# Optimization experiments

Hardware: AMD Instinct MI355X
Metric: run time of the kernel (lower is better)

## Reference

```python
import jax, jax.numpy as jnp
import numpy as np
import math

B, S, N_UNITS, D_K = 8, 2048, 1024, 512


def setup_inputs() -> dict:
    key = jax.random.key(0)
    ks = jax.random.split(key, 8)
    scale = 1.0 / math.sqrt(N_UNITS)
    query = jax.random.normal(ks[0], (B, S, N_UNITS), dtype=jnp.float32)
    k_in = jax.random.normal(ks[1], (B, S, N_UNITS), dtype=jnp.float32)
    v_in = jax.random.normal(ks[2], (B, S, N_UNITS), dtype=jnp.float32)
    # custom multiplicative mask: causal lower-triangular, broadcast over batch
    mask = jnp.broadcast_to(jnp.tril(jnp.ones((S, S), dtype=jnp.float32)), (B, S, S))
    Wq = jax.random.normal(ks[3], (N_UNITS, D_K), dtype=jnp.float32) * scale
    Wk = jax.random.normal(ks[4], (N_UNITS, D_K), dtype=jnp.float32) * scale
    Wv = jax.random.normal(ks[5], (N_UNITS, D_K), dtype=jnp.float32) * scale
    bq = jnp.zeros((D_K,), dtype=jnp.float32)
    bk = jnp.zeros((D_K,), dtype=jnp.float32)
    bv = jnp.zeros((D_K,), dtype=jnp.float32)
    return {"query": query, "key": k_in, "value": v_in, "mask": mask,
            "Wq": Wq, "bq": bq, "Wk": Wk, "bk": bk, "Wv": Wv, "bv": bv}


def reference(query, key, value, mask, Wq, bq, Wk, bk, Wv, bv):
    d_k = Wq.shape[-1]
    Q = jnp.einsum('bsn,nd->bsd', query, Wq) + bq  # [B,S,Dk]
    K = jnp.einsum('bsn,nd->bsd', key, Wk) + bk
    V = jnp.einsum('bsn,nd->bsd', value, Wv) + bv
    # scores [B,S,S]
    x_hat = jnp.einsum('bqd,bkd->bqk', Q, K) / jnp.sqrt(jnp.float32(d_k))
    # custom multiplicative mask: x*mask - 1e9*(1-mask)
    x_hat_masked = x_hat * mask - 1e9 * (1.0 - mask)
    attn = jax.nn.softmax(x_hat_masked, axis=-1)
    # dropout = 0.0 (eval mode) -> identity
    out = jnp.einsum('bqk,bkd->bqd', attn, V)
    return out
```

## Files before the change

### kernel.cpp

```cpp
#include <hip/hip_runtime.h>

typedef __bf16 bf16_t;
typedef __attribute__((ext_vector_type(4))) __bf16 bf16x4;
typedef __attribute__((ext_vector_type(8))) __bf16 bf16x8;
typedef __attribute__((ext_vector_type(4))) float f32x4;

#define B_    8
#define S_    2048
#define NU    1024
#define DK    512
#define MROWS (B_ * S_)
#define PBATCH (128 * 128 * 136)

#define WAITVM(N) asm volatile("s_waitcnt vmcnt(" #N ")" ::: "memory")
#define WAITLG    asm volatile("s_waitcnt lgkmcnt(0)" ::: "memory")
#define BAR       asm volatile("s_barrier" ::: "memory")

__device__ __forceinline__ f32x4 mfma16(bf16x8 a, bf16x8 b, f32x4 c) {
  return __builtin_amdgcn_mfma_f32_16x16x32_bf16(a, b, c, 0, 0, 0);
}

__device__ __forceinline__ void async_load16(const void* g, void* l) {
  __builtin_amdgcn_global_load_lds(
      (const __attribute__((address_space(1))) unsigned int*)g,
      (__attribute__((address_space(3))) unsigned int*)l, 16, 0, 0);
}

__device__ __forceinline__ bf16x8 cvt8(f32x4 x0, f32x4 x1) {
  bf16x8 r;
#pragma unroll
  for (int j = 0; j < 4; ++j) { r[j] = (bf16_t)x0[j]; r[j + 4] = (bf16_t)x1[j]; }
  return r;
}

__device__ __forceinline__ void stage_tile(const bf16_t* __restrict__ src,
                                           int rstride, bf16_t* dst, int k0,
                                           int tid) {
#pragma unroll
  for (int j = 0; j < 2; ++j) {
    const int g = j * 256 + tid;
    const int ln = g >> 3, c = g & 7;
    const int cs = c ^ (ln & 7);
    const int srow = 2 * ln + (cs >> 2);
    async_load16(src + (size_t)srow * rstride + k0 + (cs & 3) * 8, dst + g * 8);
  }
}

__device__ __forceinline__ void stage_tile_f32(const float* __restrict__ src,
                                               int rstride, float* dst, int k0,
                                               int tid) {
#pragma unroll
  for (int j = 0; j < 4; ++j) {
    const int g = j * 256 + tid;
    const int row = g >> 3, c = g & 7;
    const int cs = c ^ (row & 7);
    async_load16(src + (size_t)row * rstride + k0 + (cs << 2), dst + g * 4);
  }
}

__device__ __forceinline__ bf16x8 frag(const bf16_t* buf, int row, int q) {
  const int ln = row >> 1;
  const int cp = (((row & 1) << 2) | q) ^ (ln & 7);
  return *(const bf16x8*)(buf + ln * 64 + cp * 8);
}

__device__ __forceinline__ bf16x8 frag_f32(const float* buf, int row, int q) {
  const int s = row & 7;
  const f32x4 x0 = *(const f32x4*)&buf[row * 32 + (((q * 2)) ^ s) * 4];
  const f32x4 x1 = *(const f32x4*)&buf[row * 32 + (((q * 2) | 1) ^ s) * 4];
  return cvt8(x0, x1);
}

__global__ __launch_bounds__(256) void transpose_w_kernel(
    const float* __restrict__ Wq, const float* __restrict__ Wk,
    const float* __restrict__ Wv, bf16_t* __restrict__ Wt) {
  const float* W = (blockIdx.z == 0) ? Wq : (blockIdx.z == 1) ? Wk : Wv;
  bf16_t* Wo = Wt + (size_t)blockIdx.z * DK * NU;
  __shared__ float tile[32][33];
  const int t = threadIdx.x;
  const int r = t >> 5, c = t & 31;
  const int kbase = blockIdx.y * 32, nbase = blockIdx.x * 32;
#pragma unroll
  for (int i = 0; i < 4; ++i)
    tile[r + i * 8][c] = W[(size_t)(kbase + r + i * 8) * DK + nbase + c];
  __syncthreads();
#pragma unroll
  for (int i = 0; i < 4; ++i)
    Wo[(size_t)(nbase + r + i * 8) * NU + kbase + c] = (bf16_t)tile[c][r + i * 8];
}

__global__ __launch_bounds__(256, 2) void xw3_gemm_kernel(
    const float* __restrict__ q_in, const float* __restrict__ k_in,
    const float* __restrict__ v_in, const bf16_t* __restrict__ Wt,
    const float* __restrict__ bq, const float* __restrict__ bk,
    const float* __restrict__ bv, bf16_t* __restrict__ Qo,
    bf16_t* __restrict__ Ko, bf16_t* __restrict__ Vt) {
  const int bx = blockIdx.x;
  const int z = bx >> 9;
  const int t = bx & 511;
  const int m0 = (t & 127) * 128;
  const int n0 = (t >> 7) * 128;
  const float* X = (z == 0) ? q_in : (z == 1) ? k_in : v_in;
  const float* bias = (z == 0) ? bq : (z == 1) ? bk : bv;

  const int tid = threadIdx.x;
  const int wave = tid >> 6, lane = tid & 63;
  const int l16 = lane & 15, quad = lane >> 4;
  const int wm = (wave >> 1) * 64, wn = (wave & 1) * 64;

  __shared__ __align__(16) unsigned char smem[73728];
  float* ldsA = (float*)smem;
  bf16_t* ldsB = (bf16_t*)(smem + 49152);

  const float* Ag = X + (size_t)m0 * NU;
  const bf16_t* Bg = Wt + (size_t)z * DK * NU + (size_t)n0 * NU;

  f32x4 acc[4][4] = {};

  stage_tile_f32(Ag, NU, ldsA, 0, tid);
  stage_tile(Bg, NU, ldsB, 0, tid);
  stage_tile_f32(Ag, NU, ldsA + 4096, 32, tid);
  stage_tile(Bg, NU, ldsB + 4096, 32, tid);
  const int NS = 32;
  int cur = 0, nxt2 = 2;
  for (int ks = 0; ks < NS; ++ks) {
    if (ks + 1 < NS) { WAITVM(6); } else { WAITVM(0); }
    BAR;
    if (ks + 2 < NS) {
      stage_tile_f32(Ag, NU, ldsA + nxt2 * 4096, (ks + 2) * 32, tid);
      stage_tile(Bg, NU, ldsB + nxt2 * 4096, (ks + 2) * 32, tid);
    }
    const float* ac = ldsA + cur * 4096;
    const bf16_t* bc = ldsB + cur * 4096;
    bf16x8 af[4], bfr[4];
#pragma unroll
    for (int i = 0; i < 4; ++i) af[i] = frag_f32(ac, wm + i * 16 + l16, quad);
#pragma unroll
    for (int j = 0; j < 4; ++j) bfr[j] = frag(bc, wn + j * 16 + l16, quad);
#pragma unroll
    for (int i = 0; i < 4; ++i)
#pragma unroll
      for (int j = 0; j < 4; ++j)
        acc[i][j] = mfma16(af[i], bfr[j], acc[i][j]);
    cur = (cur + 1 == 3) ? 0 : cur + 1;
    nxt2 = (nxt2 + 1 == 3) ? 0 : nxt2 + 1;
  }

  if (z != 2) {
    bf16_t* Out = (z == 0) ? Qo : Ko;
#pragma unroll
    for (int j = 0; j < 4; ++j) {
      const int cn = n0 + wn + j * 16 + l16;
      const float bz = bias[cn];
#pragma unroll
      for (int i = 0; i < 4; ++i) {
        const int rm = m0 + wm + i * 16 + quad * 4;
#pragma unroll
        for (int r = 0; r < 4; ++r)
          Out[(size_t)(rm + r) * DK + cn] = (bf16_t)(acc[i][j][r] + bz);
      }
    }
  } else {
    bf16_t* Ts = (bf16_t*)smem;
    BAR;
#pragma unroll
    for (int j = 0; j < 4; ++j) {
      const int cnl = wn + j * 16 + l16;
      const float bz = bias[n0 + cnl];
#pragma unroll
      for (int i = 0; i < 4; ++i) {
        const int rs = wm + i * 16 + quad * 4;
        bf16x4 tv;
#pragma unroll
        for (int r = 0; r < 4; ++r) tv[r] = (bf16_t)(acc[i][j][r] + bz);
        *(bf16x4*)&Ts[cnl * 136 + rs] = tv;
      }
    }
    WAITLG; BAR;
    const int bb2 = m0 >> 11, sl = m0 & 2047;
    const int row = tid >> 1, half = tid & 1;
    bf16_t* dst = Vt + ((size_t)bb2 * DK + n0 + row) * S_ + sl + half * 64;
    const bf16_t* sp = &Ts[row * 136 + half * 64];
#pragma unroll
    for (int k = 0; k < 8; ++k)
      *(bf16x8*)(dst + k * 8) = *(const bf16x8*)(sp + k * 8);
  }
}

__global__ __launch_bounds__(256) void zerol_kernel(float* __restrict__ L) {
  ((f32x4*)L)[blockIdx.x * 256 + threadIdx.x] = f32x4{0.f, 0.f, 0.f, 0.f};
}

__global__ __launch_bounds__(256, 3) void qk_p_kernel(
    const bf16_t* __restrict__ Q, const bf16_t* __restrict__ K,
    bf16_t* __restrict__ P, float* __restrict__ L) {
  const int bx = blockIdx.x;
  const int b = bx & 7;
  const int t = bx >> 3;
  int mt = 0;
  while (((mt + 1) * (mt + 2)) / 2 <= t) ++mt;
  const int nt = t - (mt * (mt + 1)) / 2;
  const int klen = (mt + 1) * 128;

  const int tid = threadIdx.x;
  const int wave = tid >> 6, lane = tid & 63;
  const int l16 = lane & 15, quad = lane >> 4;
  const int wm = (wave >> 1) * 64, wn = (wave & 1) * 64;

  __shared__ __align__(16) unsigned char smem[49152];
  bf16_t* lds = (bf16_t*)smem;

  const bf16_t* Ag = Q + (size_t)(b * S_ + mt * 128) * DK;
  const bf16_t* Bg = K + (size_t)(b * S_ + nt * 128) * DK;

  f32x4 acc[4][4] = {};

  stage_tile(Ag, DK, lds, 0, tid);
  stage_tile(Bg, DK, lds + 12288, 0, tid);
  stage_tile(Ag, DK, lds + 4096, 32, tid);
  stage_tile(Bg, DK, lds + 16384, 32, tid);
  const int NS = 16;
  int cur = 0, nxt2 = 2;
  for (int ks = 0; ks < NS; ++ks) {
    if (ks + 1 < NS) { WAITVM(4); } else { WAITVM(0); }
    BAR;
    if (ks + 2 < NS) {
      stage_tile(Ag, DK, lds + nxt2 * 4096, (ks + 2) * 32, tid);
      stage_tile(Bg, DK, lds + 12288 + nxt2 * 4096, (ks + 2) * 32, tid);
    }
    const bf16_t* ac = lds + cur * 4096;
    const bf16_t* bc = lds + 12288 + cur * 4096;
    bf16x8 af[4], bfr[4];
#pragma unroll
    for (int i = 0; i < 4; ++i) af[i] = frag(ac, wm + i * 16 + l16, quad);
#pragma unroll
    for (int j = 0; j < 4; ++j) bfr[j] = frag(bc, wn + j * 16 + l16, quad);
#pragma unroll
    for (int i = 0; i < 4; ++i)
#pragma unroll
      for (int j = 0; j < 4; ++j)
        acc[i][j] = mfma16(af[i], bfr[j], acc[i][j]);
    cur = (cur + 1 == 3) ? 0 : cur + 1;
    nxt2 = (nxt2 + 1 == 3) ? 0 : nxt2 + 1;
  }

  const float scale = 0.04419417382415922f;
  bf16_t* Pt = P + (size_t)b * PBATCH + (size_t)8192 * mt * (mt + 1);
  float* Lb = L + b * S_ + mt * 128;
#pragma unroll
  for (int i = 0; i < 4; ++i) {
#pragma unroll
    for (int r = 0; r < 4; ++r) {
      const int lrow = wm + i * 16 + quad * 4 + r;
      const int srow = mt * 128 + lrow;
      float rsum = 0.f;
#pragma unroll
      for (int j = 0; j < 4; ++j) {
        const int scol = nt * 128 + wn + j * 16 + l16;
        const float p =
            (scol > srow) ? 0.f : __expf(acc[i][j][r] * scale - 10.0f);
        rsum += p;
        Pt[(size_t)lrow * klen + scol] = (bf16_t)p;
      }
#pragma unroll
      for (int off = 8; off >= 1; off >>= 1)
        rsum += __shfl_xor(rsum, off, 64);
      if (l16 == 0) atomicAdd(&Lb[lrow], rsum);
    }
  }
}

__global__ __launch_bounds__(256, 3) void pv_kernel(
    const bf16_t* __restrict__ P, const bf16_t* __restrict__ Vt,
    const float* __restrict__ L, float* __restrict__ Out) {
  const int bx = blockIdx.x;
  const int b = bx & 7;
  const int u = bx >> 3;
  const int mt = 15 - (u >> 2);
  const int d0 = (u & 3) * 128;
  const int klen = (mt + 1) * 128;
  const int NS = (mt + 1) * 4;

  const int tid = threadIdx.x;
  const int wave = tid >> 6, lane = tid & 63;
  const int l16 = lane & 15, quad = lane >> 4;
  const int wm = (wave >> 1) * 64, wn = (wave & 1) * 64;

  __shared__ __align__(16) unsigned char smem[49152];
  bf16_t* lds = (bf16_t*)smem;

  const bf16_t* Ag = P + (size_t)b * PBATCH + (size_t)8192 * mt * (mt + 1);
  const bf16_t* Bg = Vt + ((size_t)b * DK + d0) * S_;

  f32x4 acc[4][4] = {};

  stage_tile(Ag, klen, lds, 0, tid);
  stage_tile(Bg, S_, lds + 12288, 0, tid);
  stage_tile(Ag, klen, lds + 4096, 32, tid);
  stage_tile(Bg, S_, lds + 16384, 32, tid);
  int cur = 0, nxt2 = 2;
  for (int ks = 0; ks < NS; ++ks) {
    if (ks + 1 < NS) { WAITVM(4); } else { WAITVM(0); }
    BAR;
    if (ks + 2 < NS) {
      stage_tile(Ag, klen, lds + nxt2 * 4096, (ks + 2) * 32, tid);
      stage_tile(Bg, S_, lds + 12288 + nxt2 * 4096, (ks + 2) * 32, tid);
    }
    const bf16_t* ac = lds + cur * 4096;
    const bf16_t* bc = lds + 12288 + cur * 4096;
    bf16x8 af[4], bfr[4];
#pragma unroll
    for (int i = 0; i < 4; ++i) af[i] = frag(ac, wm + i * 16 + l16, quad);
#pragma unroll
    for (int j = 0; j < 4; ++j) bfr[j] = frag(bc, wn + j * 16 + l16, quad);
#pragma unroll
    for (int i = 0; i < 4; ++i)
#pragma unroll
      for (int j = 0; j < 4; ++j)
        acc[i][j] = mfma16(af[i], bfr[j], acc[i][j]);
    cur = (cur + 1 == 3) ? 0 : cur + 1;
    nxt2 = (nxt2 + 1 == 3) ? 0 : nxt2 + 1;
  }

  const int m0 = b * S_ + mt * 128;
#pragma unroll
  for (int i = 0; i < 4; ++i) {
#pragma unroll
    for (int r = 0; r < 4; ++r) {
      const int grow = m0 + wm + i * 16 + quad * 4 + r;
      const float inv = 1.0f / L[grow];
      float* orow = Out + (size_t)grow * DK + d0;
#pragma unroll
      for (int j = 0; j < 4; ++j)
        orow[wn + j * 16 + l16] = acc[i][j][r] * inv;
    }
  }
}

extern "C" void kernel_launch(void* const* d_in, const int* in_sizes, int n_in,
                              void* d_out, int out_size, void* d_ws, size_t ws_size,
                              hipStream_t stream) {
  const float* query = (const float*)d_in[0];
  const float* key_i = (const float*)d_in[1];
  const float* value = (const float*)d_in[2];
  const float* Wq = (const float*)d_in[4];
  const float* bq = (const float*)d_in[5];
  const float* Wk = (const float*)d_in[6];
  const float* bk = (const float*)d_in[7];
  const float* Wv = (const float*)d_in[8];
  const float* bv = (const float*)d_in[9];
  float* out = (float*)d_out;

  bf16_t* Wt = (bf16_t*)d_ws;
  bf16_t* Qw = Wt + (size_t)3 * DK * NU;
  bf16_t* Kw = Qw + (size_t)MROWS * DK;
  bf16_t* Vw = Kw + (size_t)MROWS * DK;
  bf16_t* Pw = Vw + (size_t)MROWS * DK;
  float* Lw = (float*)(Pw + (size_t)B_ * PBATCH);

  transpose_w_kernel<<<dim3(16, 32, 3), 256, 0, stream>>>(Wq, Wk, Wv, Wt);
  zerol_kernel<<<16, 256, 0, stream>>>(Lw);
  xw3_gemm_kernel<<<1536, 256, 0, stream>>>(query, key_i, value, Wt, bq, bk,
                                            bv, Qw, Kw, Vw);
  qk_p_kernel<<<1088, 256, 0, stream>>>(Qw, Kw, Pw, Lw);
  pv_kernel<<<512, 256, 0, stream>>>(Pw, Vw, Lw, out);
}
```

Before: 440.9 us.

## Switch GEMMs to double buffering for occupancy and replace atomic row-sum with partials

All three GEMM kernels drop from triple-buffered LDS staging (prefetch depth two) to double buffering (prefetch depth one). This shrinks shared memory so launch bounds can allow one more block per CU. Separately, the softmax row-sum atomics and the zeroing kernel are replaced by per-tile partial sums written to workspace, which pv_kernel reduces into LDS before normalising. The risk is that the shallower prefetch now waits on vmcnt(0) every step, exposing more memory latency per iteration.

New measurement: 444.0 us. Within noise of the previous version (+0.7%).

```diff
diff --git a/kernel.cpp b/kernel.cpp
--- a/kernel.cpp
+++ b/kernel.cpp
@@ -89,7 +89,7 @@
     Wo[(size_t)(nbase + r + i * 8) * NU + kbase + c] = (bf16_t)tile[c][r + i * 8];
 }
 
-__global__ __launch_bounds__(256, 2) void xw3_gemm_kernel(
+__global__ __launch_bounds__(256, 3) void xw3_gemm_kernel(
     const float* __restrict__ q_in, const float* __restrict__ k_in,
     const float* __restrict__ v_in, const bf16_t* __restrict__ Wt,
     const float* __restrict__ bq, const float* __restrict__ bk,
@@ -108,9 +108,9 @@
   const int l16 = lane & 15, quad = lane >> 4;
   const int wm = (wave >> 1) * 64, wn = (wave & 1) * 64;
 
-  __shared__ __align__(16) unsigned char smem[73728];
+  __shared__ __align__(16) unsigned char smem[49152];
   float* ldsA = (float*)smem;
-  bf16_t* ldsB = (bf16_t*)(smem + 49152);
+  bf16_t* ldsB = (bf16_t*)(smem + 32768);
 
   const float* Ag = X + (size_t)m0 * NU;
   const bf16_t* Bg = Wt + (size_t)z * DK * NU + (size_t)n0 * NU;
@@ -119,19 +119,16 @@
 
   stage_tile_f32(Ag, NU, ldsA, 0, tid);
   stage_tile(Bg, NU, ldsB, 0, tid);
-  stage_tile_f32(Ag, NU, ldsA + 4096, 32, tid);
-  stage_tile(Bg, NU, ldsB + 4096, 32, tid);
   const int NS = 32;
-  int cur = 0, nxt2 = 2;
   for (int ks = 0; ks < NS; ++ks) {
-    if (ks + 1 < NS) { WAITVM(6); } else { WAITVM(0); }
+    WAITVM(0);
     BAR;
-    if (ks + 2 < NS) {
-      stage_tile_f32(Ag, NU, ldsA + nxt2 * 4096, (ks + 2) * 32, tid);
-      stage_tile(Bg, NU, ldsB + nxt2 * 4096, (ks + 2) * 32, tid);
-    }
-    const float* ac = ldsA + cur * 4096;
-    const bf16_t* bc = ldsB + cur * 4096;
+    if (ks + 1 < NS) {
+      stage_tile_f32(Ag, NU, ldsA + ((ks + 1) & 1) * 4096, (ks + 1) * 32, tid);
+      stage_tile(Bg, NU, ldsB + ((ks + 1) & 1) * 4096, (ks + 1) * 32, tid);
+    }
+    const float* ac = ldsA + (ks & 1) * 4096;
+    const bf16_t* bc = ldsB + (ks & 1) * 4096;
     bf16x8 af[4], bfr[4];
 #pragma unroll
     for (int i = 0; i < 4; ++i) af[i] = frag_f32(ac, wm + i * 16 + l16, quad);
@@ -142,8 +139,6 @@
 #pragma unroll
       for (int j = 0; j < 4; ++j)
         acc[i][j] = mfma16(af[i], bfr[j], acc[i][j]);
-    cur = (cur + 1 == 3) ? 0 : cur + 1;
-    nxt2 = (nxt2 + 1 == 3) ? 0 : nxt2 + 1;
   }
 
   if (z != 2) {
@@ -187,13 +182,9 @@
   }
 }
 
-__global__ __launch_bounds__(256) void zerol_kernel(float* __restrict__ L) {
-  ((f32x4*)L)[blockIdx.x * 256 + threadIdx.x] = f32x4{0.f, 0.f, 0.f, 0.f};
-}
-
-__global__ __launch_bounds__(256, 3) void qk_p_kernel(
+__global__ __launch_bounds__(256, 4) void qk_p_kernel(
     const bf16_t* __restrict__ Q, const bf16_t* __restrict__ K,
-    bf16_t* __restrict__ P, float* __restrict__ L) {
+    bf16_t* __restrict__ P, float* __restrict__ Lp) {
   const int bx = blockIdx.x;
   const int b = bx & 7;
   const int t = bx >> 3;
@@ -207,29 +198,27 @@
   const int l16 = lane & 15, quad = lane >> 4;
   const int wm = (wave >> 1) * 64, wn = (wave & 1) * 64;
 
-  __shared__ __align__(16) unsigned char smem[49152];
-  bf16_t* lds = (bf16_t*)smem;
+  __shared__ __align__(16) unsigned char smem[32768];
+  bf16_t* ldsA = (bf16_t*)smem;
+  bf16_t* ldsB = (bf16_t*)(smem + 16384);
 
   const bf16_t* Ag = Q + (size_t)(b * S_ + mt * 128) * DK;
   const bf16_t* Bg = K + (size_t)(b * S_ + nt * 128) * DK;
 
   f32x4 acc[4][4] = {};
 
-  stage_tile(Ag, DK, lds, 0, tid);
-  stage_tile(Bg, DK, lds + 12288, 0, tid);
-  stage_tile(Ag, DK, lds + 4096, 32, tid);
-  stage_tile(Bg, DK, lds + 16384, 32, tid);
+  stage_tile(Ag, DK, ldsA, 0, tid);
+  stage_tile(Bg, DK, ldsB, 0, tid);
   const int NS = 16;
-  int cur = 0, nxt2 = 2;
   for (int ks = 0; ks < NS; ++ks) {
-    if (ks + 1 < NS) { WAITVM(4); } else { WAITVM(0); }
+    WAITVM(0);
     BAR;
-    if (ks + 2 < NS) {
-      stage_tile(Ag, DK, lds + nxt2 * 4096, (ks + 2) * 32, tid);
-      stage_tile(Bg, DK, lds + 12288 + nxt2 * 4096, (ks + 2) * 32, tid);
-    }
-    const bf16_t* ac = lds + cur * 4096;
-    const bf16_t* bc = lds + 12288 + cur * 4096;
+    if (ks + 1 < NS) {
+      stage_tile(Ag, DK, ldsA + ((ks + 1) & 1) * 4096, (ks + 1) * 32, tid);
+      stage_tile(Bg, DK, ldsB + ((ks + 1) & 1) * 4096, (ks + 1) * 32, tid);
+    }
+    const bf16_t* ac = ldsA + (ks & 1) * 4096;
+    const bf16_t* bc = ldsB + (ks & 1) * 4096;
     bf16x8 af[4], bfr[4];
 #pragma unroll
     for (int i = 0; i < 4; ++i) af[i] = frag(ac, wm + i * 16 + l16, quad);
@@ -240,13 +229,11 @@
 #pragma unroll
       for (int j = 0; j < 4; ++j)
         acc[i][j] = mfma16(af[i], bfr[j], acc[i][j]);
-    cur = (cur + 1 == 3) ? 0 : cur + 1;
-    nxt2 = (nxt2 + 1 == 3) ? 0 : nxt2 + 1;
   }
 
   const float scale = 0.04419417382415922f;
   bf16_t* Pt = P + (size_t)b * PBATCH + (size_t)8192 * mt * (mt + 1);
-  float* Lb = L + b * S_ + mt * 128;
+  float* Lph = Lp + ((size_t)(b * 136 + t) * 2 + (wn >> 6)) * 128;
 #pragma unroll
   for (int i = 0; i < 4; ++i) {
 #pragma unroll
@@ -265,14 +252,14 @@
 #pragma unroll
       for (int off = 8; off >= 1; off >>= 1)
         rsum += __shfl_xor(rsum, off, 64);
-      if (l16 == 0) atomicAdd(&Lb[lrow], rsum);
-    }
-  }
-}
-
-__global__ __launch_bounds__(256, 3) void pv_kernel(
+      if (l16 == 0) Lph[lrow] = rsum;
+    }
+  }
+}
+
+__global__ __launch_bounds__(256, 4) void pv_kernel(
     const bf16_t* __restrict__ P, const bf16_t* __restrict__ Vt,
-    const float* __restrict__ L, float* __restrict__ Out) {
+    const float* __restrict__ Lp, float* __restrict__ Out) {
   const int bx = blockIdx.x;
   const int b = bx & 7;
   const int u = bx >> 3;
@@ -286,28 +273,27 @@
   const int l16 = lane & 15, quad = lane >> 4;
   const int wm = (wave >> 1) * 64, wn = (wave & 1) * 64;
 
-  __shared__ __align__(16) unsigned char smem[49152];
-  bf16_t* lds = (bf16_t*)smem;
+  __shared__ __align__(16) unsigned char smem[33280];
+  bf16_t* ldsA = (bf16_t*)smem;
+  bf16_t* ldsB = (bf16_t*)(smem + 16384);
+  float* Ls = (float*)(smem + 32768);
 
   const bf16_t* Ag = P + (size_t)b * PBATCH + (size_t)8192 * mt * (mt + 1);
   const bf16_t* Bg = Vt + ((size_t)b * DK + d0) * S_;
 
   f32x4 acc[4][4] = {};
 
-  stage_tile(Ag, klen, lds, 0, tid);
-  stage_tile(Bg, S_, lds + 12288, 0, tid);
-  stage_tile(Ag, klen, lds + 4096, 32, tid);
-  stage_tile(Bg, S_, lds + 16384, 32, tid);
-  int cur = 0, nxt2 = 2;
+  stage_tile(Ag, klen, ldsA, 0, tid);
+  stage_tile(Bg, S_, ldsB, 0, tid);
   for (int ks = 0; ks < NS; ++ks) {
-    if (ks + 1 < NS) { WAITVM(4); } else { WAITVM(0); }
+    WAITVM(0);
     BAR;
-    if (ks + 2 < NS) {
-      stage_tile(Ag, klen, lds + nxt2 * 4096, (ks + 2) * 32, tid);
-      stage_tile(Bg, S_, lds + 12288 + nxt2 * 4096, (ks + 2) * 32, tid);
-    }
-    const bf16_t* ac = lds + cur * 4096;
-    const bf16_t* bc = lds + 12288 + cur * 4096;
+    if (ks + 1 < NS) {
+      stage_tile(Ag, klen, ldsA + ((ks + 1) & 1) * 4096, (ks + 1) * 32, tid);
+      stage_tile(Bg, S_, ldsB + ((ks + 1) & 1) * 4096, (ks + 1) * 32, tid);
+    }
+    const bf16_t* ac = ldsA + (ks & 1) * 4096;
+    const bf16_t* bc = ldsB + (ks & 1) * 4096;
     bf16x8 af[4], bfr[4];
 #pragma unroll
     for (int i = 0; i < 4; ++i) af[i] = frag(ac, wm + i * 16 + l16, quad);
@@ -318,18 +304,25 @@
 #pragma unroll
       for (int j = 0; j < 4; ++j)
         acc[i][j] = mfma16(af[i], bfr[j], acc[i][j]);
-    cur = (cur + 1 == 3) ? 0 : cur + 1;
-    nxt2 = (nxt2 + 1 == 3) ? 0 : nxt2 + 1;
-  }
+  }
+
+  if (tid < 128) {
+    const float* lp =
+        Lp + ((size_t)(b * 136 + (mt * (mt + 1)) / 2) * 2) * 128 + tid;
+    float s = 0.f;
+    for (int n = 0; n <= mt; ++n) s += lp[n * 256] + lp[n * 256 + 128];
+    Ls[tid] = s;
+  }
+  WAITLG; BAR;
 
   const int m0 = b * S_ + mt * 128;
 #pragma unroll
   for (int i = 0; i < 4; ++i) {
 #pragma unroll
     for (int r = 0; r < 4; ++r) {
-      const int grow = m0 + wm + i * 16 + quad * 4 + r;
-      const float inv = 1.0f / L[grow];
-      float* orow = Out + (size_t)grow * DK + d0;
+      const int lr = wm + i * 16 + quad * 4 + r;
+      const float inv = 1.0f / Ls[lr];
+      float* orow = Out + (size_t)(m0 + lr) * DK + d0;
 #pragma unroll
       for (int j = 0; j < 4; ++j)
         orow[wn + j * 16 + l16] = acc[i][j][r] * inv;
@@ -356,12 +349,11 @@
   bf16_t* Kw = Qw + (size_t)MROWS * DK;
   bf16_t* Vw = Kw + (size_t)MROWS * DK;
   bf16_t* Pw = Vw + (size_t)MROWS * DK;
-  float* Lw = (float*)(Pw + (size_t)B_ * PBATCH);
+  float* Lpw = (float*)(Pw + (size_t)B_ * PBATCH);
 
   transpose_w_kernel<<<dim3(16, 32, 3), 256, 0, stream>>>(Wq, Wk, Wv, Wt);
-  zerol_kernel<<<16, 256, 0, stream>>>(Lw);
   xw3_gemm_kernel<<<1536, 256, 0, stream>>>(query, key_i, value, Wt, bq, bk,
                                             bv, Qw, Kw, Vw);
-  qk_p_kernel<<<1088, 256, 0, stream>>>(Qw, Kw, Pw, Lw);
-  pv_kernel<<<512, 256, 0, stream>>>(Pw, Vw, Lw, out);
-}
+  qk_p_kernel<<<1088, 256, 0, stream>>>(Qw, Kw, Pw, Lpw);
+  pv_kernel<<<512, 256, 0, stream>>>(Pw, Vw, Lpw, out);
+}
```
